# Optimization experiments

Hardware: AMD Instinct MI355X
Metric: run time of the kernel (lower is better)

Reference implementation:

```python
import jax, jax.numpy as jnp
import numpy as np

N_NODES = 50000
N_EDGES = 800000
F_IN = 1024
F_MID = 256
DROP_P = 0.5


def gcn_conv(x, W, b, src, dst, norm, n_nodes):
    # x: [N, Fin], W: [Fin, Fout]. PyG GCNConv: out = scatter(norm * (xW)[src] -> dst) + b
    h = x @ W                                  # [N, Fout]
    msg = h[src] * norm[:, None]               # [E+N, Fout] gathered, normalized messages
    out = jax.ops.segment_sum(msg, dst, num_segments=n_nodes)
    return out + b


def setup_inputs() -> dict:
    key = jax.random.key(0)
    k1, k2, k3, k4, k5 = jax.random.split(key, 5)
    x = jax.random.normal(k1, (N_NODES, F_IN), dtype=jnp.float32)
    edge_index = jax.random.randint(k2, (2, N_EDGES), 0, N_NODES, dtype=jnp.int64)
    # Glorot-ish init for GCN weights
    W1 = jax.random.normal(k3, (F_IN, F_MID), dtype=jnp.float32) / np.sqrt(F_IN)
    b1 = jnp.zeros((F_MID,), dtype=jnp.float32)
    W2 = jax.random.normal(k4, (F_MID, F_IN), dtype=jnp.float32) / np.sqrt(F_MID)
    b2 = jnp.zeros((F_IN,), dtype=jnp.float32)
    return {"x": x, "edge_index": edge_index, "W1": W1, "b1": b1, "W2": W2, "b2": b2}


def reference(x, edge_index, W1, b1, W2, b2):
    n = x.shape[0]
    # add self-loops (PyG GCNConv default add_self_loops=True)
    loop = jnp.arange(n, dtype=edge_index.dtype)
    src = jnp.concatenate([edge_index[0], loop])
    dst = jnp.concatenate([edge_index[1], loop])
    # symmetric normalization D^-1/2 (A+I) D^-1/2
    deg = jax.ops.segment_sum(jnp.ones_like(dst, dtype=x.dtype), dst, num_segments=n)
    dinv = jnp.where(deg > 0, jax.lax.rsqrt(deg), 0.0)
    norm = dinv[src] * dinv[dst]               # [E+N]

    h = jax.nn.relu(gcn_conv(x, W1, b1, src, dst, norm, n))
    # F.dropout(x) default: p=0.5, training=True -> deterministic mask w/ fixed key
    keep = jax.random.bernoulli(jax.random.key(42), 1.0 - DROP_P, h.shape)
    h = jnp.where(keep, h / (1.0 - DROP_P), 0.0)
    out = gcn_conv(h, W2, b2, src, dst, norm, n)
    return out
```

## Files before the change

kernel.cpp:

```cpp
#include <hip/hip_runtime.h>
#include <hip/hip_bf16.h>

#define N_NODES 50000
#define N_EDGES 800000
#define F_IN 1024
#define F_MID 256

typedef _Float16 f16;
typedef _Float16 f16x4 __attribute__((ext_vector_type(4)));
typedef _Float16 f16x8 __attribute__((ext_vector_type(8)));
typedef float f32x4 __attribute__((ext_vector_type(4)));

__device__ __forceinline__ void glds16(const f16* g, f16* l) {
    __builtin_amdgcn_global_load_lds(
        (const __attribute__((address_space(1))) unsigned int*)g,
        (__attribute__((address_space(3))) unsigned int*)l, 16, 0, 0);
}

__device__ __forceinline__ void tf_round(unsigned &x0, unsigned &x1, int r) {
    x0 += x1;
    x1 = (x1 << r) | (x1 >> (32 - r));
    x1 ^= x0;
}

__device__ __forceinline__ int keep_mask(unsigned f) {
    const unsigned ks0 = 0u, ks1 = 42u;
    const unsigned ks2 = ks0 ^ ks1 ^ 0x1BD11BDAu;
    unsigned x0 = 0u + ks0;
    unsigned x1 = f + ks1;
    tf_round(x0,x1,13); tf_round(x0,x1,15); tf_round(x0,x1,26); tf_round(x0,x1,6);
    x0 += ks1; x1 += ks2 + 1u;
    tf_round(x0,x1,17); tf_round(x0,x1,29); tf_round(x0,x1,16); tf_round(x0,x1,24);
    x0 += ks2; x1 += ks0 + 2u;
    tf_round(x0,x1,13); tf_round(x0,x1,15); tf_round(x0,x1,26); tf_round(x0,x1,6);
    x0 += ks0; x1 += ks1 + 3u;
    tf_round(x0,x1,17); tf_round(x0,x1,29); tf_round(x0,x1,16); tf_round(x0,x1,24);
    x0 += ks1; x1 += ks2 + 4u;
    tf_round(x0,x1,13); tf_round(x0,x1,15); tf_round(x0,x1,26); tf_round(x0,x1,6);
    x0 += ks2; x1 += ks0 + 5u;
    return (((x0 ^ x1) >> 31) == 0u);
}

__device__ __forceinline__ int ld_src(const int* ei, int e, int is64) {
    return is64 ? ei[2 * e] : ei[e];
}
__device__ __forceinline__ int ld_dst(const int* ei, int e, int is64) {
    return is64 ? ei[2 * N_EDGES + 2 * e] : ei[N_EDGES + e];
}

__global__ __launch_bounds__(256) void k_prep(const float* __restrict__ W1, f16* __restrict__ W1T,
                                              const int* __restrict__ ei,
                                              int* deg, int* cursor, int* counter, int* flag) {
    const int tid = threadIdx.x;
    const int gid = blockIdx.x * 256 + tid;
    const int gstr = gridDim.x * 256;
    if (gid < N_NODES) { deg[gid] = 0; cursor[gid] = 0; }
    if (gid == 0) counter[0] = 0;
    if (blockIdx.x == 0) {
        if (tid == 0) flag[0] = 1;
        __syncthreads();
        int nz = 0;
        for (int k = tid; k < 1024; k += 256) nz |= (ei[2 * k + 1] != 0);
        if (nz) atomicAnd(flag, 0);
    }
    for (int i = gid; i < F_IN * F_MID; i += gstr) {
        int k = i >> 8, n = i & 255;
        W1T[(size_t)n * F_IN + (k ^ ((n & 7) << 3))] = (f16)W1[i];
    }
}

__global__ __launch_bounds__(256) void k_rows(const int* __restrict__ deg, float* __restrict__ dinv,
                                              int* __restrict__ rowst, int* __restrict__ counter) {
    int i = blockIdx.x * 256 + threadIdx.x;
    if (i < N_NODES) {
        dinv[i] = rsqrtf((float)(deg[i] + 1));
        rowst[i] = atomicAdd(counter, deg[i]);
    }
}

__global__ __launch_bounds__(256) void k_fill(const int* __restrict__ ei, const int* __restrict__ rowst,
                                              int* __restrict__ cursor, int* __restrict__ csr,
                                              const int* __restrict__ flag) {
    int e = blockIdx.x * 256 + threadIdx.x;
    int is64 = flag[0];
    if (e < N_EDGES) {
        int d = ld_dst(ei, e, is64);
        int pos = rowst[d] + atomicAdd(&cursor[d], 1);
        csr[pos] = ld_src(ei, e, is64);
    }
}

template<int BM, int BN, int TN, bool A16, bool C16>
__global__ __launch_bounds__(TN) void k_mfma(const void* __restrict__ Ag,
                                             const f16* __restrict__ BTg,
                                             void* __restrict__ Cg,
                                             const float* __restrict__ bias,
                                             int M, int Ntot, int K, int mainx,
                                             const int* __restrict__ ei, int* __restrict__ deg,
                                             const int* __restrict__ flag,
                                             const float* __restrict__ Wr, f16* __restrict__ WrT) {
    if ((int)blockIdx.x >= mainx) {
        const int str = (gridDim.x - mainx) * TN;
        const int t0 = (blockIdx.x - mainx) * TN + threadIdx.x;
        const int is64 = flag[0];
        for (int e = t0; e < N_EDGES; e += str)
            atomicAdd(&deg[ld_dst(ei, e, is64)], 1);
        for (int i = t0; i < F_MID * F_IN; i += str) {
            int k = i >> 10, n = i & 1023;
            WrT[(size_t)n * F_MID + (k ^ ((n & 7) << 3))] = (f16)Wr[i];
        }
        return;
    }

    constexpr int BK = 64;
    constexpr int NW = TN / 64;
    constexpr int WM = BM / 64;
    constexpr int WN = NW / WM;
    constexpr int WTN = BN / WN;
    constexpr int FN = WTN / 16;
    constexpr int SMEM_STG = (2 * BM * BK + 2 * BN * BK) * 2;
    constexpr int LDC = BN + 8;
    constexpr int SMEM_EPI = BM * LDC * (C16 ? 2 : 4);
    constexpr int SMEM_SZ = SMEM_STG > SMEM_EPI ? SMEM_STG : SMEM_EPI;
    __shared__ __align__(16) char smem[SMEM_SZ];
    f16* As_ = (f16*)smem;
    f16* Bs_ = As_ + 2 * BM * BK;

    const int tid = threadIdx.x, lane = tid & 63, wid = tid >> 6;
    const int l15 = lane & 15;
    const int wm = wid % WM, wn = wid / WM;
    const int row0 = blockIdx.x * BM, col0 = blockIdx.y * BN;

    f32x4 acc[4][FN] = {};
    const int ar = tid >> 3;
    const int ac = (tid & 7) * 8;
    f32x4 av0 = {}, av1 = {};

    const int nkt = K / BK;
    int buf = 0;

    auto stage_load = [&](int kt, int b) {
        const int k0 = kt * BK;
        if constexpr (A16) {
            const f16* A = (const f16*)Ag;
            #pragma unroll
            for (int i = wid; i < BM * BK / 512; i += NW) {
                int li = i * 512 + lane * 8;
                int r = li >> 6, c = li & 63;
                glds16(&A[(size_t)(row0 + r) * K + k0 + c], &As_[b * BM * BK + i * 512]);
            }
        } else {
            const float* A = (const float*)Ag;
            int gr = row0 + ar;
            if (gr < M) {
                av0 = __builtin_nontemporal_load((const f32x4*)&A[(size_t)gr * K + k0 + ac]);
                av1 = __builtin_nontemporal_load((const f32x4*)&A[(size_t)gr * K + k0 + ac + 4]);
            } else { av0 = (f32x4){}; av1 = (f32x4){}; }
        }
        #pragma unroll
        for (int i = wid; i < BN * BK / 512; i += NW) {
            int li = i * 512 + lane * 8;
            int r = li >> 6, c = li & 63;
            glds16(&BTg[(size_t)(col0 + r) * K + k0 + c], &Bs_[b * BN * BK + i * 512]);
        }
    };
    auto stage_write = [&](int b) {
        if constexpr (!A16) {
            f16x4 l = __builtin_convertvector(av0, f16x4);
            f16x4 h = __builtin_convertvector(av1, f16x4);
            f16x8 v = { l[0], l[1], l[2], l[3], h[0], h[1], h[2], h[3] };
            *(f16x8*)&As_[b * BM * BK + ar * 64 + (ac ^ ((ar & 7) << 3))] = v;
        }
    };

    stage_load(0, 0);
    stage_write(0);
    __syncthreads();

    for (int kt = 0; kt < nkt; ++kt) {
        if (kt + 1 < nkt) stage_load(kt + 1, buf ^ 1);
        #pragma unroll
        for (int ks = 0; ks < 2; ++ks) {
            const int cc = ks * 32 + (lane >> 4) * 8;
            f16x8 af[4], bf[FN];
            #pragma unroll
            for (int m = 0; m < 4; ++m) {
                int r = wm * 64 + m * 16 + l15;
                af[m] = *(const f16x8*)&As_[buf * BM * BK + r * 64 + (cc ^ ((r & 7) << 3))];
            }
            #pragma unroll
            for (int n = 0; n < FN; ++n) {
                int r = wn * WTN + n * 16 + l15;
                bf[n] = *(const f16x8*)&Bs_[buf * BN * BK + r * 64 + (cc ^ ((r & 7) << 3))];
            }
            #pragma unroll
            for (int m = 0; m < 4; ++m)
                #pragma unroll
                for (int n = 0; n < FN; ++n)
                    acc[m][n] = __builtin_amdgcn_mfma_f32_16x16x32_f16(af[m], bf[n], acc[m][n], 0, 0, 0);
        }
        if (kt + 1 < nkt) stage_write(buf ^ 1);
        __syncthreads();
        buf ^= 1;
    }

    if constexpr (C16) {
        f16* CT = (f16*)smem;
        #pragma unroll
        for (int m = 0; m < 4; ++m)
            #pragma unroll
            for (int j = 0; j < 4; ++j) {
                const int rl = wm * 64 + m * 16 + (lane >> 4) * 4 + j;
                #pragma unroll
                for (int n = 0; n < FN; ++n)
                    CT[rl * LDC + wn * WTN + n * 16 + l15] = (f16)acc[m][n][j];
            }
        __syncthreads();
        f16* C = (f16*)Cg;
        constexpr int NCH = BM * BN / 8;
        #pragma unroll
        for (int ci = tid; ci < NCH; ci += TN) {
            const int r = ci / (BN / 8), c = (ci % (BN / 8)) * 8;
            const int gr = row0 + r;
            if (gr < M) {
                f16x8 v = *(const f16x8*)&CT[r * LDC + c];
                *(f16x8*)&C[(size_t)gr * Ntot + col0 + c] = v;
            }
        }
    } else {
        float* CT = (float*)smem;
        #pragma unroll
        for (int m = 0; m < 4; ++m)
            #pragma unroll
            for (int j = 0; j < 4; ++j) {
                const int rl = wm * 64 + m * 16 + (lane >> 4) * 4 + j;
                #pragma unroll
                for (int n = 0; n < FN; ++n)
                    CT[rl * LDC + wn * WTN + n * 16 + l15] = acc[m][n][j];
            }
        __syncthreads();
        float* C = (float*)Cg;
        constexpr int NCH = BM * BN / 4;
        #pragma unroll
        for (int ci = tid; ci < NCH; ci += TN) {
            const int r = ci / (BN / 4), c = (ci % (BN / 4)) * 4;
            const int gr = row0 + r;
            if (gr < M) {
                f32x4 v = *(const f32x4*)&CT[r * LDC + c];
                v += *(const f32x4*)&bias[col0 + c];
                __builtin_nontemporal_store(v, (f32x4*)&C[(size_t)gr * Ntot + col0 + c]);
            }
        }
    }
}

template<int POST, int SWZ, int SCALED_IN>
__global__ __launch_bounds__(256) void k_agg16(const f16* __restrict__ hin,
                                               f16* __restrict__ hout,
                                               const int* __restrict__ csr,
                                               const int* __restrict__ rowst,
                                               const int* __restrict__ deg,
                                               const float* __restrict__ dinv,
                                               const float* __restrict__ bias) {
    const int wid = threadIdx.x >> 6;
    const int lane = threadIdx.x & 63;
    const int row = blockIdx.x * 4 + wid;
    const int start = rowst[row];
    const int cnt = deg[row];
    const int ch = lane * 4;
    const float di = dinv[row];

    f32x4 acc = __builtin_convertvector(*(const f16x4*)&hin[(size_t)row * F_MID + ch], f32x4);
    if (!SCALED_IN) acc *= di;
    int k = 0;
    for (; k + 4 <= cnt; k += 4) {
        const int s0 = csr[start + k], s1 = csr[start + k + 1];
        const int s2 = csr[start + k + 2], s3 = csr[start + k + 3];
        f16x4 v0 = *(const f16x4*)&hin[(size_t)s0 * F_MID + ch];
        f16x4 v1 = *(const f16x4*)&hin[(size_t)s1 * F_MID + ch];
        f16x4 v2 = *(const f16x4*)&hin[(size_t)s2 * F_MID + ch];
        f16x4 v3 = *(const f16x4*)&hin[(size_t)s3 * F_MID + ch];
        if (SCALED_IN) {
            acc += __builtin_convertvector(v0, f32x4) + __builtin_convertvector(v1, f32x4)
                 + __builtin_convertvector(v2, f32x4) + __builtin_convertvector(v3, f32x4);
        } else {
            acc += dinv[s0] * __builtin_convertvector(v0, f32x4)
                 + dinv[s1] * __builtin_convertvector(v1, f32x4)
                 + dinv[s2] * __builtin_convertvector(v2, f32x4)
                 + dinv[s3] * __builtin_convertvector(v3, f32x4);
        }
    }
    for (; k < cnt; ++k) {
        const int s = csr[start + k];
        f32x4 v = __builtin_convertvector(*(const f16x4*)&hin[(size_t)s * F_MID + ch], f32x4);
        acc += SCALED_IN ? v : dinv[s] * v;
    }
    acc *= di;

    if (POST) {
        const unsigned f0 = (unsigned)row * F_MID + (unsigned)ch;
        #pragma unroll
        for (int j = 0; j < 4; ++j) {
            float t = acc[j] + bias[ch + j];
            t = fmaxf(t, 0.0f);
            t = keep_mask(f0 + j) ? t * 2.0f : 0.0f;
            acc[j] = t * di;
        }
    }
    const int oc = SWZ ? (ch ^ ((row & 7) << 3)) : ch;
    *(f16x4*)&hout[(size_t)row * F_MID + oc] = __builtin_convertvector(acc, f16x4);
}

extern "C" void kernel_launch(void* const* d_in, const int* in_sizes, int n_in,
                              void* d_out, int out_size, void* d_ws, size_t ws_size,
                              hipStream_t stream) {
    const float* x  = (const float*)d_in[0];
    const int*   ei = (const int*)d_in[1];
    const float* W1 = (const float*)d_in[2];
    const float* b1 = (const float*)d_in[3];
    const float* W2 = (const float*)d_in[4];
    const float* b2 = (const float*)d_in[5];
    float* out = (float*)d_out;

    f16* h0 = (f16*)out;
    f16* h1s = h0 + (size_t)N_NODES * F_MID;

    f16*   h2agg = (f16*)d_ws;
    f16*   W1T   = h2agg + (size_t)(N_NODES + 64) * F_MID;
    f16*   W2T   = W1T + (size_t)F_MID * F_IN;
    float* dinv  = (float*)(W2T + (size_t)F_IN * F_MID);
    int*   deg   = (int*)(dinv + N_NODES);
    int*   rowst = deg + N_NODES;
    int*   cursor= rowst + N_NODES;
    int*   csr   = cursor + N_NODES;
    int*   counter = csr + N_EDGES;
    int*   flag    = counter + 1;

    k_prep<<<256, 256, 0, stream>>>(W1, W1T, ei, deg, cursor, counter, flag);

    {
        const int mainx = (N_NODES + 63) / 64;
        dim3 grid(mainx + 240, 1);
        k_mfma<64, 256, 512, false, true><<<grid, 512, 0, stream>>>(
            (const void*)x, W1T, (void*)h0, nullptr, N_NODES, F_MID, F_IN,
            mainx, ei, deg, flag, W2, W2T);
    }

    k_rows<<<(N_NODES + 255) / 256, 256, 0, stream>>>(deg, dinv, rowst, counter);
    k_fill<<<(N_EDGES + 255) / 256, 256, 0, stream>>>(ei, rowst, cursor, csr, flag);

    k_agg16<1, 0, 0><<<N_NODES / 4, 256, 0, stream>>>(h0, h1s, csr, rowst, deg, dinv, b1);
    k_agg16<0, 1, 1><<<N_NODES / 4, 256, 0, stream>>>(h1s, h2agg, csr, rowst, deg, dinv, nullptr);

    {
        const int mainx = (N_NODES + 63) / 64;
        dim3 grid(mainx, 4);
        k_mfma<64, 256, 512, true, false><<<grid, 512, 0, stream>>>(
            (const void*)h2agg, W2T, (void*)out, b2, N_NODES, F_IN, F_MID,
            mainx, ei, deg, flag, W2, W2T);
    }
}
```

Measured before the change: 344.2 us.

## Rewrite MFMA GEMM mainloop as 4-stage BK=32 pipeline with explicit waitcnts

The GEMM main loop moves from a double-buffered BK=64 scheme to a four-slot ring with BK=32. Loads are issued three tiles ahead, and hand-placed s_waitcnt and s_barrier calls replace __syncthreads. K becomes a template parameter so the loop fully unrolls, launch bounds request 4 blocks per CU, and the smem swizzle changes to match the 32-wide rows. The A tile for the fp16 GEMM now goes through registers instead of global_load_lds. The aggregation kernel's gather loop is unrolled from 4 to 8 edges for more memory-level parallelism, and its output swizzle is dropped. The manual waitcnt counts are fragile and assume a fixed count of outstanding loads, and the smaller K-step doubles the number of barriers.

After: 369.7 us. 7.4% more time.

```diff
diff --git a/kernel.cpp b/kernel.cpp
--- a/kernel.cpp
+++ b/kernel.cpp
@@ -65,7 +65,7 @@
     }
     for (int i = gid; i < F_IN * F_MID; i += gstr) {
         int k = i >> 8, n = i & 255;
-        W1T[(size_t)n * F_IN + (k ^ ((n & 7) << 3))] = (f16)W1[i];
+        W1T[(size_t)n * F_IN + (k ^ ((n & 3) << 3))] = (f16)W1[i];
     }
 }
 
@@ -90,15 +90,15 @@
     }
 }
 
-template<int BM, int BN, int TN, bool A16, bool C16>
-__global__ __launch_bounds__(TN) void k_mfma(const void* __restrict__ Ag,
-                                             const f16* __restrict__ BTg,
-                                             void* __restrict__ Cg,
-                                             const float* __restrict__ bias,
-                                             int M, int Ntot, int K, int mainx,
-                                             const int* __restrict__ ei, int* __restrict__ deg,
-                                             const int* __restrict__ flag,
-                                             const float* __restrict__ Wr, f16* __restrict__ WrT) {
+template<int BM, int BN, int TN, int K, bool A16, bool C16>
+__global__ __launch_bounds__(TN, 4) void k_mfma(const void* __restrict__ Ag,
+                                                const f16* __restrict__ BTg,
+                                                void* __restrict__ Cg,
+                                                const float* __restrict__ bias,
+                                                int M, int Ntot, int mainx,
+                                                const int* __restrict__ ei, int* __restrict__ deg,
+                                                const int* __restrict__ flag,
+                                                const float* __restrict__ Wr, f16* __restrict__ WrT) {
     if ((int)blockIdx.x >= mainx) {
         const int str = (gridDim.x - mainx) * TN;
         const int t0 = (blockIdx.x - mainx) * TN + threadIdx.x;
@@ -107,102 +107,125 @@
             atomicAdd(&deg[ld_dst(ei, e, is64)], 1);
         for (int i = t0; i < F_MID * F_IN; i += str) {
             int k = i >> 10, n = i & 1023;
-            WrT[(size_t)n * F_MID + (k ^ ((n & 7) << 3))] = (f16)Wr[i];
+            WrT[(size_t)n * F_MID + (k ^ ((n & 3) << 3))] = (f16)Wr[i];
         }
         return;
     }
 
-    constexpr int BK = 64;
+    constexpr int BK = 32;
+    constexpr int NKT = K / BK;
+    static_assert(NKT % 4 == 0 && NKT >= 8, "pipeline needs NKT multiple of 4");
     constexpr int NW = TN / 64;
-    constexpr int WM = BM / 64;
-    constexpr int WN = NW / WM;
-    constexpr int WTN = BN / WN;
+    constexpr int WTN = BN / NW;
     constexpr int FN = WTN / 16;
-    constexpr int SMEM_STG = (2 * BM * BK + 2 * BN * BK) * 2;
+    constexpr int ASLOT = BM * BK;
+    constexpr int BSLOT = BN * BK;
+    constexpr int BCH = BSLOT / 512 / NW;
+    constexpr int SMEM_STG = (4 * ASLOT + 4 * BSLOT) * 2;
     constexpr int LDC = BN + 8;
     constexpr int SMEM_EPI = BM * LDC * (C16 ? 2 : 4);
     constexpr int SMEM_SZ = SMEM_STG > SMEM_EPI ? SMEM_STG : SMEM_EPI;
     __shared__ __align__(16) char smem[SMEM_SZ];
     f16* As_ = (f16*)smem;
-    f16* Bs_ = As_ + 2 * BM * BK;
+    f16* Bs_ = As_ + 4 * ASLOT;
 
     const int tid = threadIdx.x, lane = tid & 63, wid = tid >> 6;
-    const int l15 = lane & 15;
-    const int wm = wid % WM, wn = wid / WM;
+    const int l15 = lane & 15, g8 = (lane >> 4) * 8;
     const int row0 = blockIdx.x * BM, col0 = blockIdx.y * BN;
+    const int ar = tid >> 3;
+    const int ac = (tid & 7) * 4;
 
     f32x4 acc[4][FN] = {};
-    const int ar = tid >> 3;
-    const int ac = (tid & 7) * 8;
-    f32x4 av0 = {}, av1 = {};
-
-    const int nkt = K / BK;
-    int buf = 0;
-
-    auto stage_load = [&](int kt, int b) {
-        const int k0 = kt * BK;
-        if constexpr (A16) {
-            const f16* A = (const f16*)Ag;
-            #pragma unroll
-            for (int i = wid; i < BM * BK / 512; i += NW) {
-                int li = i * 512 + lane * 8;
-                int r = li >> 6, c = li & 63;
-                glds16(&A[(size_t)(row0 + r) * K + k0 + c], &As_[b * BM * BK + i * 512]);
-            }
-        } else {
-            const float* A = (const float*)Ag;
-            int gr = row0 + ar;
-            if (gr < M) {
-                av0 = __builtin_nontemporal_load((const f32x4*)&A[(size_t)gr * K + k0 + ac]);
-                av1 = __builtin_nontemporal_load((const f32x4*)&A[(size_t)gr * K + k0 + ac + 4]);
-            } else { av0 = (f32x4){}; av1 = (f32x4){}; }
-        }
-        #pragma unroll
-        for (int i = wid; i < BN * BK / 512; i += NW) {
-            int li = i * 512 + lane * 8;
-            int r = li >> 6, c = li & 63;
-            glds16(&BTg[(size_t)(col0 + r) * K + k0 + c], &Bs_[b * BN * BK + i * 512]);
-        }
-    };
-    auto stage_write = [&](int b) {
-        if constexpr (!A16) {
-            f16x4 l = __builtin_convertvector(av0, f16x4);
-            f16x4 h = __builtin_convertvector(av1, f16x4);
-            f16x8 v = { l[0], l[1], l[2], l[3], h[0], h[1], h[2], h[3] };
-            *(f16x8*)&As_[b * BM * BK + ar * 64 + (ac ^ ((ar & 7) << 3))] = v;
-        }
-    };
-
-    stage_load(0, 0);
-    stage_write(0);
+    f32x4 av0q = {}, av1q = {}, av2q = {}, av3q = {};
+    f16x4 av0h = {}, av1h = {}, av2h = {}, av3h = {};
+
+#define ISSUE(T, S) do {                                                            \
+    const int k0_ = (T) * BK;                                                       \
+    const int gr_ = row0 + ar;                                                      \
+    if constexpr (A16) {                                                            \
+        const f16* A_ = (const f16*)Ag;                                             \
+        av##S##h = (gr_ < M) ? *(const f16x4*)&A_[(size_t)gr_ * K + k0_ + ac]       \
+                             : (f16x4){};                                           \
+    } else {                                                                        \
+        const float* A_ = (const float*)Ag;                                         \
+        av##S##q = (gr_ < M) ? __builtin_nontemporal_load(                          \
+                                   (const f32x4*)&A_[(size_t)gr_ * K + k0_ + ac])   \
+                             : (f32x4){};                                           \
+    }                                                                               \
+    _Pragma("unroll")                                                               \
+    for (int j_ = 0; j_ < BCH; ++j_) {                                              \
+        int ci_ = wid * BCH + j_;                                                   \
+        int li_ = ci_ * 512 + lane * 8;                                             \
+        int r_ = li_ >> 5, c_ = li_ & 31;                                           \
+        glds16(&BTg[(size_t)(col0 + r_) * K + k0_ + c_], &Bs_[(S) * BSLOT + ci_ * 512]); \
+    }                                                                               \
+} while (0)
+
+#define AWRITE(S) do {                                                              \
+    f16x4 h_;                                                                       \
+    if constexpr (A16) h_ = av##S##h;                                               \
+    else h_ = __builtin_convertvector(av##S##q, f16x4);                             \
+    *(f16x4*)&As_[(S) * ASLOT + ar * BK + (ac ^ ((ar & 3) << 3))] = h_;             \
+} while (0)
+
+#define COMPUTE(S) do {                                                             \
+    f16x8 af_[4], bf_[FN];                                                          \
+    _Pragma("unroll")                                                               \
+    for (int m_ = 0; m_ < 4; ++m_) {                                                \
+        int r_ = m_ * 16 + l15;                                                     \
+        af_[m_] = *(const f16x8*)&As_[(S) * ASLOT + r_ * BK + (g8 ^ ((r_ & 3) << 3))]; \
+    }                                                                               \
+    _Pragma("unroll")                                                               \
+    for (int n_ = 0; n_ < FN; ++n_) {                                               \
+        int r_ = wid * WTN + n_ * 16 + l15;                                         \
+        bf_[n_] = *(const f16x8*)&Bs_[(S) * BSLOT + r_ * BK + (g8 ^ ((r_ & 3) << 3))]; \
+    }                                                                               \
+    _Pragma("unroll")                                                               \
+    for (int m_ = 0; m_ < 4; ++m_)                                                  \
+        _Pragma("unroll")                                                           \
+        for (int n_ = 0; n_ < FN; ++n_)                                             \
+            acc[m_][n_] = __builtin_amdgcn_mfma_f32_16x16x32_f16(af_[m_], bf_[n_], acc[m_][n_], 0, 0, 0); \
+} while (0)
+
+#define PBAR() do { __builtin_amdgcn_sched_barrier(0); __builtin_amdgcn_s_barrier(); \
+                    __builtin_amdgcn_sched_barrier(0); } while (0)
+#define VMW6() asm volatile("s_waitcnt vmcnt(6) lgkmcnt(0)" ::: "memory")
+#define VMW3() asm volatile("s_waitcnt vmcnt(3) lgkmcnt(0)" ::: "memory")
+#define VMW0() asm volatile("s_waitcnt vmcnt(0) lgkmcnt(0)" ::: "memory")
+
+#define STEP(T, RD, WR, IS) do {                                                    \
+    if ((T) + 3 < NKT) ISSUE((T) + 3, IS);                                          \
+    COMPUTE(RD);                                                                    \
+    if ((T) + 1 < NKT) AWRITE(WR);                                                  \
+    if ((T) < NKT - 3) VMW6();                                                      \
+    else if ((T) == NKT - 3) VMW3();                                                \
+    else if ((T) == NKT - 2) VMW0();                                                \
+    if ((T) < NKT - 1) PBAR();                                                      \
+} while (0)
+
+    ISSUE(0, 0); ISSUE(1, 1); ISSUE(2, 2);
+    AWRITE(0);
+    VMW6(); PBAR();
+
+#pragma unroll
+    for (int g = 0; g < NKT / 4; ++g) {
+        const int t0 = g * 4;
+        STEP(t0 + 0, 0, 1, 3);
+        STEP(t0 + 1, 1, 2, 0);
+        STEP(t0 + 2, 2, 3, 1);
+        STEP(t0 + 3, 3, 0, 2);
+    }
+    VMW0();
     __syncthreads();
 
-    for (int kt = 0; kt < nkt; ++kt) {
-        if (kt + 1 < nkt) stage_load(kt + 1, buf ^ 1);
-        #pragma unroll
-        for (int ks = 0; ks < 2; ++ks) {
-            const int cc = ks * 32 + (lane >> 4) * 8;
-            f16x8 af[4], bf[FN];
-            #pragma unroll
-            for (int m = 0; m < 4; ++m) {
-                int r = wm * 64 + m * 16 + l15;
-                af[m] = *(const f16x8*)&As_[buf * BM * BK + r * 64 + (cc ^ ((r & 7) << 3))];
-            }
-            #pragma unroll
-            for (int n = 0; n < FN; ++n) {
-                int r = wn * WTN + n * 16 + l15;
-                bf[n] = *(const f16x8*)&Bs_[buf * BN * BK + r * 64 + (cc ^ ((r & 7) << 3))];
-            }
-            #pragma unroll
-            for (int m = 0; m < 4; ++m)
-                #pragma unroll
-                for (int n = 0; n < FN; ++n)
-                    acc[m][n] = __builtin_amdgcn_mfma_f32_16x16x32_f16(af[m], bf[n], acc[m][n], 0, 0, 0);
-        }
-        if (kt + 1 < nkt) stage_write(buf ^ 1);
-        __syncthreads();
-        buf ^= 1;
-    }
+#undef ISSUE
+#undef AWRITE
+#undef COMPUTE
+#undef PBAR
+#undef VMW6
+#undef VMW3
+#undef VMW0
+#undef STEP
 
     if constexpr (C16) {
         f16* CT = (f16*)smem;
@@ -210,10 +233,10 @@
         for (int m = 0; m < 4; ++m)
             #pragma unroll
             for (int j = 0; j < 4; ++j) {
-                const int rl = wm * 64 + m * 16 + (lane >> 4) * 4 + j;
+                const int rl = m * 16 + (lane >> 4) * 4 + j;
                 #pragma unroll
                 for (int n = 0; n < FN; ++n)
-                    CT[rl * LDC + wn * WTN + n * 16 + l15] = (f16)acc[m][n][j];
+                    CT[rl * LDC + wid * WTN + n * 16 + l15] = (f16)acc[m][n][j];
             }
         __syncthreads();
         f16* C = (f16*)Cg;
@@ -233,10 +256,10 @@
         for (int m = 0; m < 4; ++m)
             #pragma unroll
             for (int j = 0; j < 4; ++j) {
-                const int rl = wm * 64 + m * 16 + (lane >> 4) * 4 + j;
+                const int rl = m * 16 + (lane >> 4) * 4 + j;
                 #pragma unroll
                 for (int n = 0; n < FN; ++n)
-                    CT[rl * LDC + wn * WTN + n * 16 + l15] = acc[m][n][j];
+                    CT[rl * LDC + wid * WTN + n * 16 + l15] = acc[m][n][j];
             }
         __syncthreads();
         float* C = (float*)Cg;
@@ -254,7 +277,7 @@
     }
 }
 
-template<int POST, int SWZ, int SCALED_IN>
+template<int POST, int SCALED_IN>
 __global__ __launch_bounds__(256) void k_agg16(const f16* __restrict__ hin,
                                                f16* __restrict__ hout,
                                                const int* __restrict__ csr,
@@ -273,21 +296,19 @@
     f32x4 acc = __builtin_convertvector(*(const f16x4*)&hin[(size_t)row * F_MID + ch], f32x4);
     if (!SCALED_IN) acc *= di;
     int k = 0;
-    for (; k + 4 <= cnt; k += 4) {
-        const int s0 = csr[start + k], s1 = csr[start + k + 1];
-        const int s2 = csr[start + k + 2], s3 = csr[start + k + 3];
-        f16x4 v0 = *(const f16x4*)&hin[(size_t)s0 * F_MID + ch];
-        f16x4 v1 = *(const f16x4*)&hin[(size_t)s1 * F_MID + ch];
-        f16x4 v2 = *(const f16x4*)&hin[(size_t)s2 * F_MID + ch];
-        f16x4 v3 = *(const f16x4*)&hin[(size_t)s3 * F_MID + ch];
+    for (; k + 8 <= cnt; k += 8) {
+        int s[8];
+        f16x4 v[8];
+        #pragma unroll
+        for (int u = 0; u < 8; ++u) s[u] = csr[start + k + u];
+        #pragma unroll
+        for (int u = 0; u < 8; ++u) v[u] = *(const f16x4*)&hin[(size_t)s[u] * F_MID + ch];
         if (SCALED_IN) {
-            acc += __builtin_convertvector(v0, f32x4) + __builtin_convertvector(v1, f32x4)
-                 + __builtin_convertvector(v2, f32x4) + __builtin_convertvector(v3, f32x4);
+            #pragma unroll
+            for (int u = 0; u < 8; ++u) acc += __builtin_convertvector(v[u], f32x4);
         } else {
-            acc += dinv[s0] * __builtin_convertvector(v0, f32x4)
-                 + dinv[s1] * __builtin_convertvector(v1, f32x4)
-                 + dinv[s2] * __builtin_convertvector(v2, f32x4)
-                 + dinv[s3] * __builtin_convertvector(v3, f32x4);
+            #pragma unroll
+            for (int u = 0; u < 8; ++u) acc += dinv[s[u]] * __builtin_convertvector(v[u], f32x4);
         }
     }
     for (; k < cnt; ++k) {
@@ -307,8 +328,7 @@
             acc[j] = t * di;
         }
     }
-    const int oc = SWZ ? (ch ^ ((row & 7) << 3)) : ch;
-    *(f16x4*)&hout[(size_t)row * F_MID + oc] = __builtin_convertvector(acc, f16x4);
+    *(f16x4*)&hout[(size_t)row * F_MID + ch] = __builtin_convertvector(acc, f16x4);
 }
 
 extern "C" void kernel_launch(void* const* d_in, const int* in_sizes, int n_in,
@@ -341,22 +361,22 @@
     {
         const int mainx = (N_NODES + 63) / 64;
         dim3 grid(mainx + 240, 1);
-        k_mfma<64, 256, 512, false, true><<<grid, 512, 0, stream>>>(
-            (const void*)x, W1T, (void*)h0, nullptr, N_NODES, F_MID, F_IN,
+        k_mfma<64, 256, 512, 1024, false, true><<<grid, 512, 0, stream>>>(
+            (const void*)x, W1T, (void*)h0, nullptr, N_NODES, F_MID,
             mainx, ei, deg, flag, W2, W2T);
     }
 
     k_rows<<<(N_NODES + 255) / 256, 256, 0, stream>>>(deg, dinv, rowst, counter);
     k_fill<<<(N_EDGES + 255) / 256, 256, 0, stream>>>(ei, rowst, cursor, csr, flag);
 
-    k_agg16<1, 0, 0><<<N_NODES / 4, 256, 0, stream>>>(h0, h1s, csr, rowst, deg, dinv, b1);
-    k_agg16<0, 1, 1><<<N_NODES / 4, 256, 0, stream>>>(h1s, h2agg, csr, rowst, deg, dinv, nullptr);
+    k_agg16<1, 0><<<N_NODES / 4, 256, 0, stream>>>(h0, h1s, csr, rowst, deg, dinv, b1);
+    k_agg16<0, 1><<<N_NODES / 4, 256, 0, stream>>>(h1s, h2agg, csr, rowst, deg, dinv, nullptr);
 
     {
         const int mainx = (N_NODES + 63) / 64;
         dim3 grid(mainx, 4);
-        k_mfma<64, 256, 512, true, false><<<grid, 512, 0, stream>>>(
-            (const void*)h2agg, W2T, (void*)out, b2, N_NODES, F_IN, F_MID,
+        k_mfma<64, 256, 512, 256, true, false><<<grid, 512, 0, stream>>>(
+            (const void*)h2agg, W2T, (void*)out, b2, N_NODES, F_IN,
             mainx, ei, deg, flag, W2, W2T);
     }
 }
```

## Single-buffer MFMA GEMM with compile-time K, larger BK, whole-A preload

Applied to the files above, without the earlier changes.

Makes K and BK template parameters so the k-loop fully unrolls, and raises BK to 128 for the first GEMM. The A/B double buffering is replaced by single-buffered LDS with an extra barrier per k-step. For the second GEMM the whole 64x256 f16 A tile is loaded into LDS once. The aim is to cut loop overhead and LDS footprint, which may raise occupancy, but global loads now overlap less with MFMA compute because of the added syncs.

Result: slower. 378.5 us (+10.0%).

```diff
diff --git a/kernel.cpp b/kernel.cpp
--- a/kernel.cpp
+++ b/kernel.cpp
@@ -90,12 +90,12 @@
     }
 }
 
-template<int BM, int BN, int TN, bool A16, bool C16>
+template<int BM, int BN, int TN, int K, int BK, bool A16, bool C16>
 __global__ __launch_bounds__(TN) void k_mfma(const void* __restrict__ Ag,
                                              const f16* __restrict__ BTg,
                                              void* __restrict__ Cg,
                                              const float* __restrict__ bias,
-                                             int M, int Ntot, int K, int mainx,
+                                             int M, int Ntot, int mainx,
                                              const int* __restrict__ ei, int* __restrict__ deg,
                                              const int* __restrict__ flag,
                                              const float* __restrict__ Wr, f16* __restrict__ WrT) {
@@ -112,96 +112,117 @@
         return;
     }
 
-    constexpr int BK = 64;
+    static_assert(BM == 64 && BN == 256 && TN == 512, "tile fixed");
+    constexpr int NKT = K / BK;
     constexpr int NW = TN / 64;
-    constexpr int WM = BM / 64;
-    constexpr int WN = NW / WM;
-    constexpr int WTN = BN / WN;
+    constexpr int WTN = BN / NW;
     constexpr int FN = WTN / 16;
-    constexpr int SMEM_STG = (2 * BM * BK + 2 * BN * BK) * 2;
+    constexpr int ALDS = A16 ? BM * K : BM * BK;
+    constexpr int BLDS = BN * BK;
+    constexpr int SMEM_STG = (ALDS + BLDS) * 2;
     constexpr int LDC = BN + 8;
     constexpr int SMEM_EPI = BM * LDC * (C16 ? 2 : 4);
     constexpr int SMEM_SZ = SMEM_STG > SMEM_EPI ? SMEM_STG : SMEM_EPI;
     __shared__ __align__(16) char smem[SMEM_SZ];
     f16* As_ = (f16*)smem;
-    f16* Bs_ = As_ + 2 * BM * BK;
+    f16* Bs_ = As_ + ALDS;
 
     const int tid = threadIdx.x, lane = tid & 63, wid = tid >> 6;
-    const int l15 = lane & 15;
-    const int wm = wid % WM, wn = wid / WM;
+    const int l15 = lane & 15, g8 = (lane >> 4) * 8;
     const int row0 = blockIdx.x * BM, col0 = blockIdx.y * BN;
 
+    constexpr int BCH = BLDS / 512 / NW;
+    auto gldsB = [&](int kt) {
+        const int k0 = kt * BK;
+        #pragma unroll
+        for (int j = 0; j < BCH; ++j) {
+            int ci = wid * BCH + j;
+            int li = ci * 512 + lane * 8;
+            int r = li / BK, c = li % BK;
+            glds16(&BTg[(size_t)(col0 + r) * K + k0 + c], &Bs_[ci * 512]);
+        }
+    };
+
+    const int ar = tid >> 3;
+    const int ac = (tid & 7) * 16;
+    f32x4 av[4];
+    auto loadA = [&](int kt) {
+        const float* A = (const float*)Ag;
+        const int gr = row0 + ar;
+        const int k0 = kt * BK;
+        if (gr < M) {
+            #pragma unroll
+            for (int u = 0; u < 4; ++u)
+                av[u] = __builtin_nontemporal_load((const f32x4*)&A[(size_t)gr * K + k0 + ac + u * 4]);
+        } else {
+            #pragma unroll
+            for (int u = 0; u < 4; ++u) av[u] = (f32x4){};
+        }
+    };
+    auto awrite = [&]() {
+        f16x4 a0 = __builtin_convertvector(av[0], f16x4);
+        f16x4 a1 = __builtin_convertvector(av[1], f16x4);
+        f16x4 a2 = __builtin_convertvector(av[2], f16x4);
+        f16x4 a3 = __builtin_convertvector(av[3], f16x4);
+        f16x8 lo = { a0[0],a0[1],a0[2],a0[3], a1[0],a1[1],a1[2],a1[3] };
+        f16x8 hi = { a2[0],a2[1],a2[2],a2[3], a3[0],a3[1],a3[2],a3[3] };
+        const int sw = (ar & 7) << 3;
+        *(f16x8*)&As_[ar * BK + (ac ^ sw)] = lo;
+        *(f16x8*)&As_[ar * BK + ((ac + 8) ^ sw)] = hi;
+    };
+
     f32x4 acc[4][FN] = {};
-    const int ar = tid >> 3;
-    const int ac = (tid & 7) * 8;
-    f32x4 av0 = {}, av1 = {};
-
-    const int nkt = K / BK;
-    int buf = 0;
-
-    auto stage_load = [&](int kt, int b) {
-        const int k0 = kt * BK;
-        if constexpr (A16) {
-            const f16* A = (const f16*)Ag;
-            #pragma unroll
-            for (int i = wid; i < BM * BK / 512; i += NW) {
-                int li = i * 512 + lane * 8;
-                int r = li >> 6, c = li & 63;
-                glds16(&A[(size_t)(row0 + r) * K + k0 + c], &As_[b * BM * BK + i * 512]);
-            }
-        } else {
-            const float* A = (const float*)Ag;
-            int gr = row0 + ar;
-            if (gr < M) {
-                av0 = __builtin_nontemporal_load((const f32x4*)&A[(size_t)gr * K + k0 + ac]);
-                av1 = __builtin_nontemporal_load((const f32x4*)&A[(size_t)gr * K + k0 + ac + 4]);
-            } else { av0 = (f32x4){}; av1 = (f32x4){}; }
-        }
-        #pragma unroll
-        for (int i = wid; i < BN * BK / 512; i += NW) {
-            int li = i * 512 + lane * 8;
-            int r = li >> 6, c = li & 63;
-            glds16(&BTg[(size_t)(col0 + r) * K + k0 + c], &Bs_[b * BN * BK + i * 512]);
-        }
-    };
-    auto stage_write = [&](int b) {
-        if constexpr (!A16) {
-            f16x4 l = __builtin_convertvector(av0, f16x4);
-            f16x4 h = __builtin_convertvector(av1, f16x4);
-            f16x8 v = { l[0], l[1], l[2], l[3], h[0], h[1], h[2], h[3] };
-            *(f16x8*)&As_[b * BM * BK + ar * 64 + (ac ^ ((ar & 7) << 3))] = v;
-        }
-    };
-
-    stage_load(0, 0);
-    stage_write(0);
+
+    if constexpr (A16) {
+        constexpr int ACH = ALDS / 512 / NW;
+        #pragma unroll
+        for (int j = 0; j < ACH; ++j) {
+            int ci = wid * ACH + j;
+            int li = ci * 512 + lane * 8;
+            int r = li / K, c = li % K;
+            glds16(&((const f16*)Ag)[(size_t)(row0 + r) * K + c], &As_[ci * 512]);
+        }
+    } else {
+        loadA(0);
+        awrite();
+    }
+    gldsB(0);
     __syncthreads();
 
-    for (int kt = 0; kt < nkt; ++kt) {
-        if (kt + 1 < nkt) stage_load(kt + 1, buf ^ 1);
-        #pragma unroll
-        for (int ks = 0; ks < 2; ++ks) {
-            const int cc = ks * 32 + (lane >> 4) * 8;
-            f16x8 af[4], bf[FN];
-            #pragma unroll
-            for (int m = 0; m < 4; ++m) {
-                int r = wm * 64 + m * 16 + l15;
-                af[m] = *(const f16x8*)&As_[buf * BM * BK + r * 64 + (cc ^ ((r & 7) << 3))];
-            }
-            #pragma unroll
-            for (int n = 0; n < FN; ++n) {
-                int r = wn * WTN + n * 16 + l15;
-                bf[n] = *(const f16x8*)&Bs_[buf * BN * BK + r * 64 + (cc ^ ((r & 7) << 3))];
-            }
-            #pragma unroll
-            for (int m = 0; m < 4; ++m)
-                #pragma unroll
-                for (int n = 0; n < FN; ++n)
-                    acc[m][n] = __builtin_amdgcn_mfma_f32_16x16x32_f16(af[m], bf[n], acc[m][n], 0, 0, 0);
-        }
-        if (kt + 1 < nkt) stage_write(buf ^ 1);
+    #pragma unroll
+    for (int kt = 0; kt < NKT; ++kt) {
+        if constexpr (!A16) { if (kt + 1 < NKT) loadA(kt + 1); }
+        {
+            constexpr int ALD = A16 ? K : BK;
+            const int kbase = A16 ? kt * BK : 0;
+            #pragma unroll
+            for (int ks = 0; ks < BK / 32; ++ks) {
+                const int clA = kbase + ks * 32 + g8;
+                const int clB = ks * 32 + g8;
+                f16x8 af[4], bf[FN];
+                #pragma unroll
+                for (int m = 0; m < 4; ++m) {
+                    int r = m * 16 + l15;
+                    af[m] = *(const f16x8*)&As_[r * ALD + (clA ^ ((r & 7) << 3))];
+                }
+                #pragma unroll
+                for (int n = 0; n < FN; ++n) {
+                    int r = wid * WTN + n * 16 + l15;
+                    bf[n] = *(const f16x8*)&Bs_[r * BK + (clB ^ ((r & 7) << 3))];
+                }
+                #pragma unroll
+                for (int m = 0; m < 4; ++m)
+                    #pragma unroll
+                    for (int n = 0; n < FN; ++n)
+                        acc[m][n] = __builtin_amdgcn_mfma_f32_16x16x32_f16(af[m], bf[n], acc[m][n], 0, 0, 0);
+            }
+        }
         __syncthreads();
-        buf ^= 1;
+        if (kt + 1 < NKT) {
+            if constexpr (!A16) awrite();
+            gldsB(kt + 1);
+            __syncthreads();
+        }
     }
 
     if constexpr (C16) {
@@ -210,10 +231,10 @@
         for (int m = 0; m < 4; ++m)
             #pragma unroll
             for (int j = 0; j < 4; ++j) {
-                const int rl = wm * 64 + m * 16 + (lane >> 4) * 4 + j;
+                const int rl = m * 16 + (lane >> 4) * 4 + j;
                 #pragma unroll
                 for (int n = 0; n < FN; ++n)
-                    CT[rl * LDC + wn * WTN + n * 16 + l15] = (f16)acc[m][n][j];
+                    CT[rl * LDC + wid * WTN + n * 16 + l15] = (f16)acc[m][n][j];
             }
         __syncthreads();
         f16* C = (f16*)Cg;
@@ -233,10 +254,10 @@
         for (int m = 0; m < 4; ++m)
             #pragma unroll
             for (int j = 0; j < 4; ++j) {
-                const int rl = wm * 64 + m * 16 + (lane >> 4) * 4 + j;
+                const int rl = m * 16 + (lane >> 4) * 4 + j;
                 #pragma unroll
                 for (int n = 0; n < FN; ++n)
-                    CT[rl * LDC + wn * WTN + n * 16 + l15] = acc[m][n][j];
+                    CT[rl * LDC + wid * WTN + n * 16 + l15] = acc[m][n][j];
             }
         __syncthreads();
         float* C = (float*)Cg;
@@ -340,9 +361,9 @@
 
     {
         const int mainx = (N_NODES + 63) / 64;
-        dim3 grid(mainx + 240, 1);
-        k_mfma<64, 256, 512, false, true><<<grid, 512, 0, stream>>>(
-            (const void*)x, W1T, (void*)h0, nullptr, N_NODES, F_MID, F_IN,
+        dim3 grid(mainx + 242, 1);
+        k_mfma<64, 256, 512, 1024, 128, false, true><<<grid, 512, 0, stream>>>(
+            (const void*)x, W1T, (void*)h0, nullptr, N_NODES, F_MID,
             mainx, ei, deg, flag, W2, W2T);
     }
 
@@ -355,8 +376,8 @@
     {
         const int mainx = (N_NODES + 63) / 64;
         dim3 grid(mainx, 4);
-        k_mfma<64, 256, 512, true, false><<<grid, 512, 0, stream>>>(
-            (const void*)h2agg, W2T, (void*)out, b2, N_NODES, F_IN, F_MID,
+        k_mfma<64, 256, 512, 256, 64, true, false><<<grid, 512, 0, stream>>>(
+            (const void*)h2agg, W2T, (void*)out, b2, N_NODES, F_IN,
             mainx, ei, deg, flag, W2, W2T);
     }
 }
```

## Precompute dropout bitmask in GEMM side-blocks and widen aggregation to 8 channels per lane

Applied to the files above, without the earlier changes.

The Threefry-based dropout mask is no longer computed inline in the first aggregation kernel. Instead it is packed into 32-bit words by the spare blocks of the first GEMM launch, where it overlaps with the matmul, and the aggregation reads one word per lane. The aggregation kernels also switch to 16-byte f16x8 gathers with two rows per wavefront, which halves the number of load instructions per edge. The mask adds a 1.6 MB workspace buffer and extra work to the side blocks, which could lengthen the GEMM if those blocks end up on the critical path.

Measured after the change: 365.5 us. 6.2% more time.

```diff
diff --git a/kernel.cpp b/kernel.cpp
--- a/kernel.cpp
+++ b/kernel.cpp
@@ -5,11 +5,13 @@
 #define N_EDGES 800000
 #define F_IN 1024
 #define F_MID 256
+#define NMASKW (N_NODES * F_MID / 32)
 
 typedef _Float16 f16;
 typedef _Float16 f16x4 __attribute__((ext_vector_type(4)));
 typedef _Float16 f16x8 __attribute__((ext_vector_type(8)));
 typedef float f32x4 __attribute__((ext_vector_type(4)));
+typedef float f32x8 __attribute__((ext_vector_type(8)));
 
 __device__ __forceinline__ void glds16(const f16* g, f16* l) {
     __builtin_amdgcn_global_load_lds(
@@ -98,7 +100,8 @@
                                              int M, int Ntot, int K, int mainx,
                                              const int* __restrict__ ei, int* __restrict__ deg,
                                              const int* __restrict__ flag,
-                                             const float* __restrict__ Wr, f16* __restrict__ WrT) {
+                                             const float* __restrict__ Wr, f16* __restrict__ WrT,
+                                             unsigned* __restrict__ maskw) {
     if ((int)blockIdx.x >= mainx) {
         const int str = (gridDim.x - mainx) * TN;
         const int t0 = (blockIdx.x - mainx) * TN + threadIdx.x;
@@ -108,6 +111,13 @@
         for (int i = t0; i < F_MID * F_IN; i += str) {
             int k = i >> 10, n = i & 1023;
             WrT[(size_t)n * F_MID + (k ^ ((n & 7) << 3))] = (f16)Wr[i];
+        }
+        for (int w = t0; w < NMASKW; w += str) {
+            unsigned bits = 0;
+            #pragma unroll 4
+            for (int b = 0; b < 32; ++b)
+                bits |= (unsigned)keep_mask((unsigned)w * 32u + (unsigned)b) << b;
+            maskw[w] = bits;
         }
         return;
     }
@@ -261,54 +271,56 @@
                                                const int* __restrict__ rowst,
                                                const int* __restrict__ deg,
                                                const float* __restrict__ dinv,
-                                               const float* __restrict__ bias) {
+                                               const float* __restrict__ bias,
+                                               const unsigned* __restrict__ maskw) {
     const int wid = threadIdx.x >> 6;
     const int lane = threadIdx.x & 63;
-    const int row = blockIdx.x * 4 + wid;
+    const int row = blockIdx.x * 8 + wid * 2 + (lane >> 5);
     const int start = rowst[row];
     const int cnt = deg[row];
-    const int ch = lane * 4;
+    const int ch = (lane & 31) * 8;
     const float di = dinv[row];
 
-    f32x4 acc = __builtin_convertvector(*(const f16x4*)&hin[(size_t)row * F_MID + ch], f32x4);
+    f32x8 acc = __builtin_convertvector(*(const f16x8*)&hin[(size_t)row * F_MID + ch], f32x8);
     if (!SCALED_IN) acc *= di;
     int k = 0;
     for (; k + 4 <= cnt; k += 4) {
         const int s0 = csr[start + k], s1 = csr[start + k + 1];
         const int s2 = csr[start + k + 2], s3 = csr[start + k + 3];
-        f16x4 v0 = *(const f16x4*)&hin[(size_t)s0 * F_MID + ch];
-        f16x4 v1 = *(const f16x4*)&hin[(size_t)s1 * F_MID + ch];
-        f16x4 v2 = *(const f16x4*)&hin[(size_t)s2 * F_MID + ch];
-        f16x4 v3 = *(const f16x4*)&hin[(size_t)s3 * F_MID + ch];
+        f16x8 v0 = *(const f16x8*)&hin[(size_t)s0 * F_MID + ch];
+        f16x8 v1 = *(const f16x8*)&hin[(size_t)s1 * F_MID + ch];
+        f16x8 v2 = *(const f16x8*)&hin[(size_t)s2 * F_MID + ch];
+        f16x8 v3 = *(const f16x8*)&hin[(size_t)s3 * F_MID + ch];
         if (SCALED_IN) {
-            acc += __builtin_convertvector(v0, f32x4) + __builtin_convertvector(v1, f32x4)
-                 + __builtin_convertvector(v2, f32x4) + __builtin_convertvector(v3, f32x4);
+            acc += __builtin_convertvector(v0, f32x8) + __builtin_convertvector(v1, f32x8)
+                 + __builtin_convertvector(v2, f32x8) + __builtin_convertvector(v3, f32x8);
         } else {
-            acc += dinv[s0] * __builtin_convertvector(v0, f32x4)
-                 + dinv[s1] * __builtin_convertvector(v1, f32x4)
-                 + dinv[s2] * __builtin_convertvector(v2, f32x4)
-                 + dinv[s3] * __builtin_convertvector(v3, f32x4);
+            acc += dinv[s0] * __builtin_convertvector(v0, f32x8)
+                 + dinv[s1] * __builtin_convertvector(v1, f32x8)
+                 + dinv[s2] * __builtin_convertvector(v2, f32x8)
+                 + dinv[s3] * __builtin_convertvector(v3, f32x8);
         }
     }
     for (; k < cnt; ++k) {
         const int s = csr[start + k];
-        f32x4 v = __builtin_convertvector(*(const f16x4*)&hin[(size_t)s * F_MID + ch], f32x4);
+        f32x8 v = __builtin_convertvector(*(const f16x8*)&hin[(size_t)s * F_MID + ch], f32x8);
         acc += SCALED_IN ? v : dinv[s] * v;
     }
     acc *= di;
 
     if (POST) {
         const unsigned f0 = (unsigned)row * F_MID + (unsigned)ch;
-        #pragma unroll
-        for (int j = 0; j < 4; ++j) {
+        const unsigned mb = (maskw[f0 >> 5] >> (ch & 31)) & 0xFFu;
+        #pragma unroll
+        for (int j = 0; j < 8; ++j) {
             float t = acc[j] + bias[ch + j];
             t = fmaxf(t, 0.0f);
-            t = keep_mask(f0 + j) ? t * 2.0f : 0.0f;
+            t = ((mb >> j) & 1u) ? t * 2.0f : 0.0f;
             acc[j] = t * di;
         }
     }
     const int oc = SWZ ? (ch ^ ((row & 7) << 3)) : ch;
-    *(f16x4*)&hout[(size_t)row * F_MID + oc] = __builtin_convertvector(acc, f16x4);
+    *(f16x8*)&hout[(size_t)row * F_MID + oc] = __builtin_convertvector(acc, f16x8);
 }
 
 extern "C" void kernel_launch(void* const* d_in, const int* in_sizes, int n_in,
@@ -335,6 +347,7 @@
     int*   csr   = cursor + N_NODES;
     int*   counter = csr + N_EDGES;
     int*   flag    = counter + 1;
+    unsigned* maskw = (unsigned*)(flag + 1);
 
     k_prep<<<256, 256, 0, stream>>>(W1, W1T, ei, deg, cursor, counter, flag);
 
@@ -343,20 +356,20 @@
         dim3 grid(mainx + 240, 1);
         k_mfma<64, 256, 512, false, true><<<grid, 512, 0, stream>>>(
             (const void*)x, W1T, (void*)h0, nullptr, N_NODES, F_MID, F_IN,
-            mainx, ei, deg, flag, W2, W2T);
+            mainx, ei, deg, flag, W2, W2T, maskw);
     }
 
     k_rows<<<(N_NODES + 255) / 256, 256, 0, stream>>>(deg, dinv, rowst, counter);
     k_fill<<<(N_EDGES + 255) / 256, 256, 0, stream>>>(ei, rowst, cursor, csr, flag);
 
-    k_agg16<1, 0, 0><<<N_NODES / 4, 256, 0, stream>>>(h0, h1s, csr, rowst, deg, dinv, b1);
-    k_agg16<0, 1, 1><<<N_NODES / 4, 256, 0, stream>>>(h1s, h2agg, csr, rowst, deg, dinv, nullptr);
+    k_agg16<1, 0, 0><<<N_NODES / 8, 256, 0, stream>>>(h0, h1s, csr, rowst, deg, dinv, b1, maskw);
+    k_agg16<0, 1, 1><<<N_NODES / 8, 256, 0, stream>>>(h1s, h2agg, csr, rowst, deg, dinv, nullptr, maskw);
 
     {
         const int mainx = (N_NODES + 63) / 64;
         dim3 grid(mainx, 4);
         k_mfma<64, 256, 512, true, false><<<grid, 512, 0, stream>>>(
             (const void*)h2agg, W2T, (void*)out, b2, N_NODES, F_IN, F_MID,
-            mainx, ei, deg, flag, W2, W2T);
-    }
-}
+            mainx, ei, deg, flag, W2, W2T, maskw);
+    }
+}
```
